# Kernel tuning notes

Hardware: AMD Instinct MI355X
Metric: run time of the kernel (lower is better)

The kernel has to match this reference:

```python
import jax, jax.numpy as jnp
import numpy as np

B, T, D = 4, 2048, 768
H = 12
DH = D // H  # 64
SCALE = DH ** -0.5


def setup_inputs() -> dict:
    key = jax.random.key(0)
    k1, k2, k3, k4 = jax.random.split(key, 4)
    x = jax.random.normal(k1, (B, T, D), dtype=jnp.float32)
    # torch nn.Linear weights: stored [out, in], applied as x @ W.T
    Wqkv = jax.random.normal(k2, (3 * D, D), dtype=jnp.float32) * (D ** -0.5)
    Wproj = jax.random.normal(k3, (D, D), dtype=jnp.float32) * (D ** -0.5)
    bproj = jax.random.normal(k4, (D,), dtype=jnp.float32) * 0.01
    return {"x": x, "Wqkv": Wqkv, "Wproj": Wproj, "bproj": bproj}


def reference(x, Wqkv, Wproj, bproj):
    Bb, Tt, C = x.shape
    qkv = x @ Wqkv.T                       # [B,T,3D]
    q, k, v = jnp.split(qkv, 3, axis=-1)   # each [B,T,D]
    q = q.reshape(Bb, Tt, H, DH)
    k = k.reshape(Bb, Tt, H, DH)
    v = v.reshape(Bb, Tt, H, DH)
    # scores [B,H,T,T]
    att = jnp.einsum('bqhd,bkhd->bhqk', q, k) * SCALE
    causal = jnp.triu(jnp.ones((Tt, Tt), dtype=bool), k=1)
    att = jnp.where(causal, -jnp.inf, att)
    att = jax.nn.softmax(att, axis=-1)
    out = jnp.einsum('bhqk,bkhd->bqhd', att, v).reshape(Bb, Tt, C)
    return out @ Wproj.T + bproj
```

## Files before the change

kernel.cpp:

```cpp
#include <hip/hip_runtime.h>
#include <hip/hip_bf16.h>


#define BATCH  4
#define SEQ    2048
#define DMODEL 768
#define NH     12
#define DHEAD  64
static constexpr float SCALE_LOG2E = 0.125f * 1.4426950408889634f;

#define N_X  (8192 * 768)
#define N_WQ (2304 * 768)
#define N_WP (768 * 768)

typedef __bf16 v8bf __attribute__((ext_vector_type(8)));
typedef __bf16 v4bf __attribute__((ext_vector_type(4)));
typedef float  v4f  __attribute__((ext_vector_type(4)));

__device__ __forceinline__ v8bf cvt8(const float* __restrict__ p) {
    const float4 a = ((const float4*)p)[0];
    const float4 b = ((const float4*)p)[1];
    v8bf r;
    r[0] = (__bf16)a.x; r[1] = (__bf16)a.y; r[2] = (__bf16)a.z; r[3] = (__bf16)a.w;
    r[4] = (__bf16)b.x; r[5] = (__bf16)b.y; r[6] = (__bf16)b.z; r[7] = (__bf16)b.w;
    return r;
}

__device__ __forceinline__ void async_copy16(__bf16* lds, const __bf16* g) {
    __builtin_amdgcn_global_load_lds(
        (const __attribute__((address_space(1))) void*)g,
        (__attribute__((address_space(3))) void*)lds, 16, 0, 0);
}

__global__ __launch_bounds__(256) void cvt_kernel(
        const float* __restrict__ x, const float* __restrict__ Wq,
        const float* __restrict__ Wp, __bf16* __restrict__ xb,
        __bf16* __restrict__ Wqb, __bf16* __restrict__ Wpb) {
    const long e = ((long)blockIdx.x * 256 + threadIdx.x) * 8;
    const float* src;
    __bf16* dst;
    if (e < N_X)             { src = x  + e;               dst = xb  + e; }
    else if (e < N_X + N_WQ) { src = Wq + (e - N_X);        dst = Wqb + (e - N_X); }
    else                     { src = Wp + (e - N_X - N_WQ); dst = Wpb + (e - N_X - N_WQ); }
    *(v8bf*)dst = cvt8(src);
}

__global__ __launch_bounds__(256) void qkv_gemm(
        const __bf16* __restrict__ xb, const __bf16* __restrict__ Wb,
        __bf16* __restrict__ Qb, __bf16* __restrict__ Kb, __bf16* __restrict__ Vtb) {
    __shared__ __bf16 As[2][128 * 32], Bs[2][128 * 32];
    const int lane = threadIdx.x & 63, wave = threadIdx.x >> 6;
    const int i = blockIdx.x;
    const int mb = ((i & 7) << 3) | ((i >> 3) & 7);
    const int nb = i >> 6;
    const int r16 = lane & 15, quad = lane >> 4;
    const int wm = (wave >> 1) * 64, wn = (wave & 1) * 64;
    const __bf16* Asrc = xb + (size_t)mb * 128 * DMODEL;
    const __bf16* Bsrc = Wb + (size_t)nb * 128 * DMODEL;

    const int srow = wave * 16 + (lane >> 2);
    const int sg   = lane & 3;
    const int g    = sg ^ ((srow >> 1) & 3);
    const size_t soff0 = (size_t)srow * DMODEL + g * 8;
    const size_t soff1 = (size_t)(srow + 64) * DMODEL + g * 8;
    const int ld0 = wave * 512;
    const int ld1 = 2048 + wave * 512;
    const int p_rd = quad ^ ((r16 >> 1) & 3);

    async_copy16(&As[0][ld0], Asrc + soff0);
    async_copy16(&As[0][ld1], Asrc + soff1);
    async_copy16(&Bs[0][ld0], Bsrc + soff0);
    async_copy16(&Bs[0][ld1], Bsrc + soff1);

    v4f acc[4][4] = {};
    for (int c = 0; c < 24; ++c) {
        const int cur = c & 1;
        __syncthreads();
        if (c + 1 < 24) {
            const int nxt = cur ^ 1;
            const size_t k1 = (c + 1) * 32;
            async_copy16(&As[nxt][ld0], Asrc + soff0 + k1);
            async_copy16(&As[nxt][ld1], Asrc + soff1 + k1);
            async_copy16(&Bs[nxt][ld0], Bsrc + soff0 + k1);
            async_copy16(&Bs[nxt][ld1], Bsrc + soff1 + k1);
        }
        v8bf a[4], b[4];
#pragma unroll
        for (int ii = 0; ii < 4; ++ii)
            a[ii] = *(const v8bf*)&As[cur][(wm + 16 * ii + r16) * 32 + p_rd * 8];
#pragma unroll
        for (int j = 0; j < 4; ++j)
            b[j] = *(const v8bf*)&Bs[cur][(wn + 16 * j + r16) * 32 + p_rd * 8];
#pragma unroll
        for (int ii = 0; ii < 4; ++ii)
#pragma unroll
            for (int j = 0; j < 4; ++j)
                acc[ii][j] = __builtin_amdgcn_mfma_f32_16x16x32_bf16(
                    a[ii], b[j], acc[ii][j], 0, 0, 0);
    }

    const int seg = nb / 6;
    const int nl0 = (nb % 6) * 128 + wn;
#pragma unroll
    for (int j = 0; j < 4; ++j) {
        const int n = nl0 + 16 * j + r16;
        const int h = n >> 6, d = n & 63;
#pragma unroll
        for (int ii = 0; ii < 4; ++ii) {
            const int mrow = mb * 128 + wm + 16 * ii + quad * 4;
            const int bidx = mrow >> 11, t0 = mrow & (SEQ - 1);
            const size_t base = ((size_t)(bidx * NH + h)) * SEQ * DHEAD;
            if (seg == 2) {
                v4bf pk;
#pragma unroll
                for (int r = 0; r < 4; ++r) pk[r] = (__bf16)acc[ii][j][r];
                *(v4bf*)&Vtb[base + (size_t)d * SEQ + t0] = pk;
            } else if (seg == 0) {
#pragma unroll
                for (int r = 0; r < 4; ++r)
                    Qb[base + (size_t)(t0 + r) * DHEAD + d] =
                        (__bf16)(acc[ii][j][r] * SCALE_LOG2E);
            } else {
#pragma unroll
                for (int r = 0; r < 4; ++r)
                    Kb[base + (size_t)(t0 + r) * DHEAD + d] = (__bf16)acc[ii][j][r];
            }
        }
    }
}

__global__ __launch_bounds__(256, 3) void attn_kernel(
        const __bf16* __restrict__ Qb, const __bf16* __restrict__ Kb,
        const __bf16* __restrict__ Vtb, __bf16* __restrict__ attnb) {
    __shared__ __bf16 Ks[2][2][64 * 32];
    __shared__ __bf16 Vs[2][2][64 * 32];
    __shared__ __align__(16) __bf16 Pl[4][32 * 72];
    const int lane = threadIdx.x & 63;
    const int wave = threadIdx.x >> 6;
    const int bh = blockIdx.x % 48;
    const int qt = 15 - (blockIdx.x / 48);
    const int q0 = qt * 128 + wave * 32;
    const int r16 = lane & 15, quad = lane >> 4;

    const __bf16* Q  = Qb  + (size_t)bh * SEQ * DHEAD;
    const __bf16* K  = Kb  + (size_t)bh * SEQ * DHEAD;
    const __bf16* Vt = Vtb + (size_t)bh * DHEAD * SEQ;

    const int srow = wave * 16 + (lane >> 2);
    const int sg   = lane & 3;
    const int g    = sg ^ ((srow >> 1) & 3);
    const int ldw  = wave * 512;
    const int p_rd = quad ^ ((r16 >> 1) & 3);

    v8bf aq[2][2];
#pragma unroll
    for (int ii = 0; ii < 2; ++ii)
#pragma unroll
        for (int kk = 0; kk < 2; ++kk)
            aq[ii][kk] = *(const v8bf*)(Q + (size_t)(q0 + 16 * ii + r16) * DHEAD
                                          + kk * 32 + quad * 8);

    v8bf vones;
#pragma unroll
    for (int j = 0; j < 8; ++j) vones[j] = (__bf16)1.0f;

    v4f oacc[2][4] = {};
    v4f lacc[2] = {};

    const int nchunks = 2 * (qt + 1);
#pragma unroll
    for (int kk = 0; kk < 2; ++kk) {
        async_copy16(&Ks[0][kk][ldw], K + (size_t)srow * DHEAD + kk * 32 + g * 8);
        async_copy16(&Vs[0][kk][ldw], Vt + (size_t)srow * SEQ + kk * 32 + g * 8);
    }

    for (int c = 0; c < nchunks; ++c) {
        const int k0 = c * 64;
        const int cur = c & 1;
        __syncthreads();
        if (c + 1 < nchunks) {
            const int nxt = cur ^ 1;
            const int k1 = k0 + 64;
#pragma unroll
            for (int kk = 0; kk < 2; ++kk) {
                async_copy16(&Ks[nxt][kk][ldw],
                             K + (size_t)(k1 + srow) * DHEAD + kk * 32 + g * 8);
                async_copy16(&Vs[nxt][kk][ldw],
                             Vt + (size_t)srow * SEQ + k1 + kk * 32 + g * 8);
            }
        }
        v8bf bk[4][2], bv[2][4];
#pragma unroll
        for (int s = 0; s < 4; ++s)
#pragma unroll
            for (int kk = 0; kk < 2; ++kk)
                bk[s][kk] = *(const v8bf*)&Ks[cur][kk][(16 * s + r16) * 32 + p_rd * 8];
#pragma unroll
        for (int kk = 0; kk < 2; ++kk)
#pragma unroll
            for (int n = 0; n < 4; ++n)
                bv[kk][n] = *(const v8bf*)&Vs[cur][kk][(16 * n + r16) * 32 + p_rd * 8];
        if (k0 > q0 + 31) continue;

        v4f sc[2][4] = {};
#pragma unroll
        for (int kk = 0; kk < 2; ++kk)
#pragma unroll
            for (int ii = 0; ii < 2; ++ii)
#pragma unroll
                for (int s = 0; s < 4; ++s)
                    sc[ii][s] = __builtin_amdgcn_mfma_f32_16x16x32_bf16(
                        aq[ii][kk], bk[s][kk], sc[ii][s], 0, 0, 0);

        if (k0 + 63 > q0) {
#pragma unroll
            for (int ii = 0; ii < 2; ++ii)
#pragma unroll
                for (int s = 0; s < 4; ++s)
#pragma unroll
                    for (int r = 0; r < 4; ++r) {
                        const int row = q0 + 16 * ii + quad * 4 + r;
                        const int col = k0 + 16 * s + r16;
                        if (col > row) sc[ii][s][r] = -1e30f;
                    }
        }

#pragma unroll
        for (int ii = 0; ii < 2; ++ii)
#pragma unroll
            for (int s = 0; s < 4; ++s)
#pragma unroll
                for (int r = 0; r < 4; ++r)
                    sc[ii][s][r] = __builtin_exp2f(sc[ii][s][r]);

#pragma unroll
        for (int ii = 0; ii < 2; ++ii)
#pragma unroll
            for (int s = 0; s < 4; ++s)
#pragma unroll
                for (int r = 0; r < 4; ++r)
                    Pl[wave][(16 * ii + quad * 4 + r) * 72 + 16 * s + r16] =
                        (__bf16)sc[ii][s][r];
        __builtin_amdgcn_s_waitcnt(0xC07F);

        v8bf ap[2][2];
#pragma unroll
        for (int ii = 0; ii < 2; ++ii)
#pragma unroll
            for (int kk = 0; kk < 2; ++kk)
                ap[ii][kk] = *(const v8bf*)&Pl[wave][(16 * ii + r16) * 72 + kk * 32 + quad * 8];
#pragma unroll
        for (int kk = 0; kk < 2; ++kk)
#pragma unroll
            for (int ii = 0; ii < 2; ++ii) {
#pragma unroll
                for (int n = 0; n < 4; ++n)
                    oacc[ii][n] = __builtin_amdgcn_mfma_f32_16x16x32_bf16(
                        ap[ii][kk], bv[kk][n], oacc[ii][n], 0, 0, 0);
                lacc[ii] = __builtin_amdgcn_mfma_f32_16x16x32_bf16(
                    ap[ii][kk], vones, lacc[ii], 0, 0, 0);
            }
    }

    const int b = bh / NH, h = bh - b * NH;
#pragma unroll
    for (int ii = 0; ii < 2; ++ii)
#pragma unroll
        for (int r = 0; r < 4; ++r) {
            const float inv = 1.0f / lacc[ii][r];
            const int t = q0 + 16 * ii + quad * 4 + r;
#pragma unroll
            for (int n = 0; n < 4; ++n) {
                const int d = 16 * n + r16;
                attnb[((size_t)(b * SEQ + t)) * DMODEL + h * DHEAD + d] =
                    (__bf16)(oacc[ii][n][r] * inv);
            }
        }
}

__global__ __launch_bounds__(256) void proj_gemm(
        const __bf16* __restrict__ Ab, const __bf16* __restrict__ Wb,
        const float* __restrict__ bias, float* __restrict__ out) {
    __shared__ __bf16 As[2][64 * 32], Bs[2][128 * 32];
    const int lane = threadIdx.x & 63, wave = threadIdx.x >> 6;
    const int i = blockIdx.x;
    const int mb = ((i & 7) << 4) | ((i >> 3) & 15);
    const int nb = i >> 7;
    const int r16 = lane & 15, quad = lane >> 4;
    const int wm = (wave >> 1) * 32, wn = (wave & 1) * 64;
    const __bf16* Asrc = Ab + (size_t)mb * 64 * DMODEL;
    const __bf16* Bsrc = Wb + (size_t)nb * 128 * DMODEL;

    const int srow = wave * 16 + (lane >> 2);
    const int sg   = lane & 3;
    const int g    = sg ^ ((srow >> 1) & 3);
    const size_t soffA  = (size_t)srow * DMODEL + g * 8;
    const size_t soffB0 = soffA;
    const size_t soffB1 = (size_t)(srow + 64) * DMODEL + g * 8;
    const int ld0 = wave * 512;
    const int ld1 = 2048 + wave * 512;
    const int p_rd = quad ^ ((r16 >> 1) & 3);

    async_copy16(&As[0][ld0], Asrc + soffA);
    async_copy16(&Bs[0][ld0], Bsrc + soffB0);
    async_copy16(&Bs[0][ld1], Bsrc + soffB1);

    v4f acc[2][4] = {};
    for (int c = 0; c < 24; ++c) {
        const int cur = c & 1;
        __syncthreads();
        if (c + 1 < 24) {
            const int nxt = cur ^ 1;
            const size_t k1 = (c + 1) * 32;
            async_copy16(&As[nxt][ld0], Asrc + soffA + k1);
            async_copy16(&Bs[nxt][ld0], Bsrc + soffB0 + k1);
            async_copy16(&Bs[nxt][ld1], Bsrc + soffB1 + k1);
        }
        v8bf a[2], b[4];
#pragma unroll
        for (int ii = 0; ii < 2; ++ii)
            a[ii] = *(const v8bf*)&As[cur][(wm + 16 * ii + r16) * 32 + p_rd * 8];
#pragma unroll
        for (int j = 0; j < 4; ++j)
            b[j] = *(const v8bf*)&Bs[cur][(wn + 16 * j + r16) * 32 + p_rd * 8];
#pragma unroll
        for (int ii = 0; ii < 2; ++ii)
#pragma unroll
            for (int j = 0; j < 4; ++j)
                acc[ii][j] = __builtin_amdgcn_mfma_f32_16x16x32_bf16(
                    a[ii], b[j], acc[ii][j], 0, 0, 0);
    }

#pragma unroll
    for (int j = 0; j < 4; ++j) {
        const int n = nb * 128 + wn + 16 * j + r16;
        const float bv = bias[n];
#pragma unroll
        for (int ii = 0; ii < 2; ++ii) {
            const int mrow = mb * 64 + wm + 16 * ii + quad * 4;
#pragma unroll
            for (int r = 0; r < 4; ++r)
                out[(size_t)(mrow + r) * DMODEL + n] = acc[ii][j][r] + bv;
        }
    }
}

extern "C" void kernel_launch(void* const* d_in, const int* in_sizes, int n_in,
                              void* d_out, int out_size, void* d_ws, size_t ws_size,
                              hipStream_t stream) {
    const float* x     = (const float*)d_in[0];
    const float* Wqkv  = (const float*)d_in[1];
    const float* Wproj = (const float*)d_in[2];
    const float* bproj = (const float*)d_in[3];
    float* out = (float*)d_out;

    char* ws = (char*)d_ws;
    const size_t tsz = (size_t)BATCH * NH * SEQ * DHEAD * sizeof(__bf16);
    __bf16* Qb    = (__bf16*)(ws);
    __bf16* Kb    = (__bf16*)(ws + tsz);
    __bf16* Vtb   = (__bf16*)(ws + 2 * tsz);
    __bf16* xb    = (__bf16*)(ws + 3 * tsz);
    __bf16* attnb = (__bf16*)(ws + 3 * tsz);
    __bf16* Wqb   = (__bf16*)(ws + 4 * tsz);
    __bf16* Wpb   = (__bf16*)(ws + 4 * tsz + (size_t)N_WQ * 2);

    cvt_kernel<<<dim3((N_X + N_WQ + N_WP) / (8 * 256)), dim3(256), 0, stream>>>(
        x, Wqkv, Wproj, xb, Wqb, Wpb);
    qkv_gemm<<<dim3(64 * 18), dim3(256), 0, stream>>>(xb, Wqb, Qb, Kb, Vtb);
    attn_kernel<<<dim3(16 * 48), dim3(256), 0, stream>>>(Qb, Kb, Vtb, attnb);
    proj_gemm<<<dim3(128 * 6), dim3(256), 0, stream>>>(attnb, Wpb, bproj, out);
}
```

Measured before the change: 214.5 us.

## Reorder LDS reads before prefetch, load V directly, widen proj K-tile

In the QKV GEMM and attention loops, shared-memory fragment reads now come before the next chunk's async prefetch is issued. The attention kernel drops V staging through LDS and loads V^T fragments straight from global memory, only for chunks that pass the causal check. This cuts LDS use and raises the occupancy hint from 3 to 4 blocks. The projection GEMM doubles its K-tile to 64 with a new XOR swizzle and half the iterations, trading more LDS per block for fewer barriers, but uncoalesced global V loads in attention may add latency.

```diff
diff --git a/kernel.cpp b/kernel.cpp
--- a/kernel.cpp
+++ b/kernel.cpp
@@ -76,6 +76,13 @@
     for (int c = 0; c < 24; ++c) {
         const int cur = c & 1;
         __syncthreads();
+        v8bf a[4], b[4];
+#pragma unroll
+        for (int ii = 0; ii < 4; ++ii)
+            a[ii] = *(const v8bf*)&As[cur][(wm + 16 * ii + r16) * 32 + p_rd * 8];
+#pragma unroll
+        for (int j = 0; j < 4; ++j)
+            b[j] = *(const v8bf*)&Bs[cur][(wn + 16 * j + r16) * 32 + p_rd * 8];
         if (c + 1 < 24) {
             const int nxt = cur ^ 1;
             const size_t k1 = (c + 1) * 32;
@@ -84,13 +91,6 @@
             async_copy16(&Bs[nxt][ld0], Bsrc + soff0 + k1);
             async_copy16(&Bs[nxt][ld1], Bsrc + soff1 + k1);
         }
-        v8bf a[4], b[4];
-#pragma unroll
-        for (int ii = 0; ii < 4; ++ii)
-            a[ii] = *(const v8bf*)&As[cur][(wm + 16 * ii + r16) * 32 + p_rd * 8];
-#pragma unroll
-        for (int j = 0; j < 4; ++j)
-            b[j] = *(const v8bf*)&Bs[cur][(wn + 16 * j + r16) * 32 + p_rd * 8];
 #pragma unroll
         for (int ii = 0; ii < 4; ++ii)
 #pragma unroll
@@ -129,11 +129,10 @@
     }
 }
 
-__global__ __launch_bounds__(256, 3) void attn_kernel(
+__global__ __launch_bounds__(256, 4) void attn_kernel(
         const __bf16* __restrict__ Qb, const __bf16* __restrict__ Kb,
         const __bf16* __restrict__ Vtb, __bf16* __restrict__ attnb) {
     __shared__ __bf16 Ks[2][2][64 * 32];
-    __shared__ __bf16 Vs[2][2][64 * 32];
     __shared__ __align__(16) __bf16 Pl[4][32 * 72];
     const int lane = threadIdx.x & 63;
     const int wave = threadIdx.x >> 6;
@@ -169,38 +168,36 @@
 
     const int nchunks = 2 * (qt + 1);
 #pragma unroll
-    for (int kk = 0; kk < 2; ++kk) {
+    for (int kk = 0; kk < 2; ++kk)
         async_copy16(&Ks[0][kk][ldw], K + (size_t)srow * DHEAD + kk * 32 + g * 8);
-        async_copy16(&Vs[0][kk][ldw], Vt + (size_t)srow * SEQ + kk * 32 + g * 8);
-    }
 
     for (int c = 0; c < nchunks; ++c) {
         const int k0 = c * 64;
         const int cur = c & 1;
         __syncthreads();
+        v8bf bk[4][2];
+#pragma unroll
+        for (int s = 0; s < 4; ++s)
+#pragma unroll
+            for (int kk = 0; kk < 2; ++kk)
+                bk[s][kk] = *(const v8bf*)&Ks[cur][kk][(16 * s + r16) * 32 + p_rd * 8];
         if (c + 1 < nchunks) {
             const int nxt = cur ^ 1;
             const int k1 = k0 + 64;
 #pragma unroll
-            for (int kk = 0; kk < 2; ++kk) {
+            for (int kk = 0; kk < 2; ++kk)
                 async_copy16(&Ks[nxt][kk][ldw],
                              K + (size_t)(k1 + srow) * DHEAD + kk * 32 + g * 8);
-                async_copy16(&Vs[nxt][kk][ldw],
-                             Vt + (size_t)srow * SEQ + k1 + kk * 32 + g * 8);
-            }
-        }
-        v8bf bk[4][2], bv[2][4];
-#pragma unroll
-        for (int s = 0; s < 4; ++s)
-#pragma unroll
-            for (int kk = 0; kk < 2; ++kk)
-                bk[s][kk] = *(const v8bf*)&Ks[cur][kk][(16 * s + r16) * 32 + p_rd * 8];
+        }
+        if (k0 > q0 + 31) continue;
+
+        v8bf bv[2][4];
 #pragma unroll
         for (int kk = 0; kk < 2; ++kk)
 #pragma unroll
             for (int n = 0; n < 4; ++n)
-                bv[kk][n] = *(const v8bf*)&Vs[cur][kk][(16 * n + r16) * 32 + p_rd * 8];
-        if (k0 > q0 + 31) continue;
+                bv[kk][n] = *(const v8bf*)(Vt + (size_t)(16 * n + r16) * SEQ
+                                             + k0 + kk * 32 + quad * 8);
 
         v4f sc[2][4] = {};
 #pragma unroll
@@ -281,7 +278,7 @@
 __global__ __launch_bounds__(256) void proj_gemm(
         const __bf16* __restrict__ Ab, const __bf16* __restrict__ Wb,
         const float* __restrict__ bias, float* __restrict__ out) {
-    __shared__ __bf16 As[2][64 * 32], Bs[2][128 * 32];
+    __shared__ __bf16 As[2][64 * 64], Bs[2][128 * 64];
     const int lane = threadIdx.x & 63, wave = threadIdx.x >> 6;
     const int i = blockIdx.x;
     const int mb = ((i & 7) << 4) | ((i >> 3) & 15);
@@ -291,44 +288,73 @@
     const __bf16* Asrc = Ab + (size_t)mb * 64 * DMODEL;
     const __bf16* Bsrc = Wb + (size_t)nb * 128 * DMODEL;
 
-    const int srow = wave * 16 + (lane >> 2);
-    const int sg   = lane & 3;
-    const int g    = sg ^ ((srow >> 1) & 3);
-    const size_t soffA  = (size_t)srow * DMODEL + g * 8;
-    const size_t soffB0 = soffA;
-    const size_t soffB1 = (size_t)(srow + 64) * DMODEL + g * 8;
-    const int ld0 = wave * 512;
-    const int ld1 = 2048 + wave * 512;
-    const int p_rd = quad ^ ((r16 >> 1) & 3);
-
-    async_copy16(&As[0][ld0], Asrc + soffA);
-    async_copy16(&Bs[0][ld0], Bsrc + soffB0);
-    async_copy16(&Bs[0][ld1], Bsrc + soffB1);
+    const int tid = threadIdx.x;
+    const int swA = (tid + 0) >> 3;
+    (void)swA;
+    const int p8 = r16 & 7;
+
+    auto stageA = [&](int buf, int c) {
+#pragma unroll
+        for (int a = 0; a < 2; ++a) {
+            const int ub = a * 256 + wave * 64;
+            const int u = ub + lane;
+            const int row = u >> 3, gl = u & 7;
+            const int gs = gl ^ (row & 7);
+            async_copy16(&As[buf][ub * 8],
+                         Asrc + (size_t)row * DMODEL + c * 64 + gs * 8);
+        }
+    };
+    auto stageB = [&](int buf, int c) {
+#pragma unroll
+        for (int a = 0; a < 4; ++a) {
+            const int ub = a * 256 + wave * 64;
+            const int u = ub + lane;
+            const int row = u >> 3, gl = u & 7;
+            const int gs = gl ^ (row & 7);
+            async_copy16(&Bs[buf][ub * 8],
+                         Bsrc + (size_t)row * DMODEL + c * 64 + gs * 8);
+        }
+    };
+
+    stageA(0, 0);
+    stageB(0, 0);
 
     v4f acc[2][4] = {};
-    for (int c = 0; c < 24; ++c) {
+    for (int c = 0; c < 12; ++c) {
         const int cur = c & 1;
         __syncthreads();
-        if (c + 1 < 24) {
+        v8bf a[2][2], b[4][2];
+#pragma unroll
+        for (int ii = 0; ii < 2; ++ii) {
+            const int row = wm + 16 * ii + r16;
+#pragma unroll
+            for (int kk = 0; kk < 2; ++kk) {
+                const int gp = (4 * kk + quad) ^ (row & 7);
+                a[ii][kk] = *(const v8bf*)&As[cur][(row * 8 + gp) * 8];
+            }
+        }
+#pragma unroll
+        for (int j = 0; j < 4; ++j) {
+            const int row = wn + 16 * j + r16;
+#pragma unroll
+            for (int kk = 0; kk < 2; ++kk) {
+                const int gp = (4 * kk + quad) ^ (row & 7);
+                b[j][kk] = *(const v8bf*)&Bs[cur][(row * 8 + gp) * 8];
+            }
+        }
+        if (c + 1 < 12) {
             const int nxt = cur ^ 1;
-            const size_t k1 = (c + 1) * 32;
-            async_copy16(&As[nxt][ld0], Asrc + soffA + k1);
-            async_copy16(&Bs[nxt][ld0], Bsrc + soffB0 + k1);
-            async_copy16(&Bs[nxt][ld1], Bsrc + soffB1 + k1);
-        }
-        v8bf a[2], b[4];
-#pragma unroll
-        for (int ii = 0; ii < 2; ++ii)
-            a[ii] = *(const v8bf*)&As[cur][(wm + 16 * ii + r16) * 32 + p_rd * 8];
-#pragma unroll
-        for (int j = 0; j < 4; ++j)
-            b[j] = *(const v8bf*)&Bs[cur][(wn + 16 * j + r16) * 32 + p_rd * 8];
-#pragma unroll
-        for (int ii = 0; ii < 2; ++ii)
-#pragma unroll
-            for (int j = 0; j < 4; ++j)
-                acc[ii][j] = __builtin_amdgcn_mfma_f32_16x16x32_bf16(
-                    a[ii], b[j], acc[ii][j], 0, 0, 0);
+            stageA(nxt, c + 1);
+            stageB(nxt, c + 1);
+        }
+#pragma unroll
+        for (int kk = 0; kk < 2; ++kk)
+#pragma unroll
+            for (int ii = 0; ii < 2; ++ii)
+#pragma unroll
+                for (int j = 0; j < 4; ++j)
+                    acc[ii][j] = __builtin_amdgcn_mfma_f32_16x16x32_bf16(
+                        a[ii][kk], b[j][kk], acc[ii][j], 0, 0, 0);
     }
 
 #pragma unroll
```

New measurement: 302.1 us. 1.41x slower.
